# Kernel tuning notes

Hardware: AMD Instinct MI355X
Metric: run time of the kernel (lower is better)

The kernel has to match this reference:

```python
import jax, jax.numpy as jnp
import numpy as np

K = 8            # regular-rep dim (C_8), reg_dim
R_BINS = 3       # num_radii
T_BINS = 16      # num_theta
G = R_BINS * T_BINS
RADIUS = 40.0    # radius_scale
DT = 1.0
CORR = 1.0 / 128.0
SHIFT = 0.2
TWO_PI = 2.0 * np.pi

# [m,n] -> (m-n) mod K, for circulant (group-equivariant) linear maps on the regular rep
_SIDX = (np.arange(K)[:, None] - np.arange(K)[None, :]) % K


def _basis(ab):
    # learnable equivariant intertwiner rho1 <-> regular: a*u_m + b*u_m_perp
    th = jnp.arange(K, dtype=jnp.float32) * (TWO_PI / K)
    U = jnp.stack([jnp.cos(th), jnp.sin(th)], -1)       # [K,2]
    Up = jnp.stack([-jnp.sin(th), jnp.cos(th)], -1)
    return ab[0] * U + ab[1] * Up


def lift_rho1_to_reg(v, ab):
    # v [...,c,2] -> [...,c,K]
    return jnp.einsum('...ca,ma->...cm', v, _basis(ab))


def proj_reg_to_rho1(x, ab):
    # x [...,c,K] -> [...,c,2]
    return jnp.einsum('...cm,ma->...ca', x, _basis(ab))


def equi_linear_reg(x, W):
    # x [...,ci,K], W [co,ci,K]; out[...,o,m] = sum_{i,s} W[o,i,s] x[...,i,(m-s)%K]
    Wc = W[:, :, _SIDX]                                  # [co,ci,m,n]
    return jnp.einsum('...in,oimn->...om', x, Wc)


def _full_kernel(W):
    # base W [co,ci,K,R,T] -> rotated stack [K(m),co,ci,K(n),G]
    s = T_BINS // K
    kern = jnp.stack([jnp.roll(jnp.roll(W, m, axis=2), m * s, axis=4) for m in range(K)], 0)
    return kern.reshape(K, W.shape[0], W.shape[1], K, G)


def pair_bin_weights(p, mask):
    # Dense pairwise continuous-conv weights: window * bilinear polar-grid interpolation,
    # normalized by the neighbor window sum. p [B,N,2], mask [B,N] -> [B,N,N,G]
    N = p.shape[1]
    rel = p[:, None, :, :] - p[:, :, None, :]            # rel[b,i,j] = p_j - p_i
    d = jnp.sqrt(jnp.sum(rel * rel, -1) + 1e-12) / RADIUS
    window = jnp.maximum(1.0 - d * d, 0.0) ** 3          # radius cutoff + window
    wb = window * mask[:, None, :]
    wb = wb / (jnp.sum(wb, -1, keepdims=True) + 1e-6)    # neighbor normalization
    rc = jnp.clip(d * R_BINS - 0.5, 0.0, R_BINS - 1.0)
    r0 = jnp.floor(rc); wr = rc - r0
    r0i = r0.astype(jnp.int32); r1i = jnp.minimum(r0i + 1, R_BINS - 1)
    eye = jnp.eye(N, dtype=bool)[None]                   # safe atan2 at self-pairs
    rx = jnp.where(eye, 1.0, rel[..., 0]); ry = jnp.where(eye, 0.0, rel[..., 1])
    tc = (jnp.arctan2(ry, rx) % TWO_PI) / TWO_PI * T_BINS
    t0 = jnp.floor(tc); wt = tc - t0
    t0i = t0.astype(jnp.int32) % T_BINS; t1i = (t0i + 1) % T_BINS
    gs = [r0i * T_BINS + t0i, r0i * T_BINS + t1i, r1i * T_BINS + t0i, r1i * T_BINS + t1i]
    ws = [(1 - wr) * (1 - wt), (1 - wr) * wt, wr * (1 - wt), wr * wt]
    Wsum = jnp.zeros(d.shape + (G,), jnp.float32)
    for g, w in zip(gs, ws):
        Wsum = Wsum + (w * wb)[..., None] * jax.nn.one_hot(g, G, dtype=jnp.float32)
    return Wsum


def cts_conv(Wsum, feats, Wk):
    # feats [B,N,ci,K] -> [B,N,co,K]
    F = jnp.einsum('bijg,bjcn->bigcn', Wsum, feats)      # bin neighbor features onto polar grid
    return jnp.einsum('bigcn,mocng->biom', F, _full_kernel(Wk))


def mag_act(x):
    mags = jnp.sum(x * x, -1, keepdims=True) + 1e-6
    return x / mags * jax.nn.relu(mags - SHIFT)


def setup_inputs() -> dict:
    key = jax.random.key(0)
    B, N, T = 2, 512, 7
    ks = jax.random.split(key, 20)
    s = 0.05
    return {
        'p0_enc': jax.random.uniform(ks[0], (B, N, T, 2), jnp.float32) * 100.0,
        'v0_enc': jax.random.normal(ks[1], (B, N, T, 2), jnp.float32),
        'p0': jax.random.uniform(ks[2], (B, N, 2), jnp.float32) * 100.0,
        'v0': jax.random.normal(ks[3], (B, N, 2), jnp.float32),
        'a': jax.random.normal(ks[4], (B, N, 2), jnp.float32) * 0.1,
        'fluid_mask': jnp.ones((B, N), jnp.float32),
        'lift_c0': jax.random.normal(ks[5], (2,), jnp.float32) * s,
        'Wc0': jax.random.normal(ks[6], (4, 16, K, R_BINS, T_BINS), jnp.float32) * s,
        'lift_d0': jax.random.normal(ks[7], (2,), jnp.float32) * s,
        'Wd0': jax.random.normal(ks[8], (4, 16, K), jnp.float32) * s,
        'Wc1': jax.random.normal(ks[9], (8, 8, K, R_BINS, T_BINS), jnp.float32) * s,
        'Wd1': jax.random.normal(ks[10], (8, 8, K), jnp.float32) * s,
        'Wc2': jax.random.normal(ks[11], (16, 8, K, R_BINS, T_BINS), jnp.float32) * s,
        'Wd2': jax.random.normal(ks[12], (16, 8, K), jnp.float32) * s,
        'Wc3': jax.random.normal(ks[13], (8, 16, K, R_BINS, T_BINS), jnp.float32) * s,
        'Wd3': jax.random.normal(ks[14], (8, 16, K), jnp.float32) * s,
        'Wc4': jax.random.normal(ks[15], (3, 8, K, R_BINS, T_BINS), jnp.float32) * s,
        'proj_c4': jax.random.normal(ks[16], (2,), jnp.float32) * s,
        'Wd4': jax.random.normal(ks[17], (3, 8, K), jnp.float32) * s,
        'proj_d4': jax.random.normal(ks[18], (2,), jnp.float32) * s,
    }


def reference(p0_enc, v0_enc, p0, v0, a, fluid_mask,
              lift_c0, Wc0, lift_d0, Wd0, Wc1, Wd1, Wc2, Wd2,
              Wc3, Wd3, Wc4, proj_c4, Wd4, proj_d4):
    feats = jnp.concatenate([v0_enc, p0_enc], -2)        # [B,N,14,2]
    v1 = v0 + DT * a
    p1 = p0 + DT * (v0 + v1) / 2.0
    fluid_feats = jnp.concatenate([v1[:, :, None, :], p1[:, :, None, :], feats], -2)  # [B,N,16,2]
    Wsum = pair_bin_weights(p1, fluid_mask)              # shared across all conv layers
    out_conv = cts_conv(Wsum, lift_rho1_to_reg(fluid_feats, lift_c0), Wc0)
    out_dense = equi_linear_reg(lift_rho1_to_reg(fluid_feats, lift_d0), Wd0)
    output = jnp.concatenate([out_conv, out_dense], -2)  # [B,N,8,K]
    for Wc, Wd, last in ((Wc1, Wd1, False), (Wc2, Wd2, False), (Wc3, Wd3, False), (Wc4, Wd4, True)):
        in_feats = mag_act(output)
        oc = cts_conv(Wsum, in_feats, Wc)
        od = equi_linear_reg(in_feats, Wd)
        if last:
            oc = proj_reg_to_rho1(oc, proj_c4)
            od = proj_reg_to_rho1(od, proj_d4)
        new = oc + od
        if new.shape[-2] == output.shape[-2] and new.shape[-1] == output.shape[-1]:
            new = new + output
        output = new
    pos_correction = CORR * output                       # [B,N,3,2]
    p_corr = p1 + pos_correction[..., 0, :]
    v_corr = (p_corr - p0) / DT
    m_matrix = pos_correction[..., 1:, :]                # [B,N,2,2]
    return p_corr, v_corr, m_matrix
```

## Files before the change

### kernel.cpp

```cpp
#include <hip/hip_runtime.h>

#define NPART 1024
#define NNB   512
#define EMAX  2048

__global__ void prep_kernel(const float* __restrict__ p0_enc, const float* __restrict__ v0_enc,
                            const float* __restrict__ p0, const float* __restrict__ v0,
                            const float* __restrict__ a, const float* __restrict__ liftc,
                            const float* __restrict__ liftd,
                            float* __restrict__ featsC, float* __restrict__ Fbuf,
                            float* __restrict__ p1out)
{
    int p = blockIdx.x;
    int t = threadIdx.x;
    int c = t >> 3, m = t & 7;
    float v0x = v0[p*2+0], v0y = v0[p*2+1];
    float ax  = a[p*2+0],  ay  = a[p*2+1];
    float p0x = p0[p*2+0], p0y = p0[p*2+1];
    float v1x = v0x + ax, v1y = v0y + ay;
    float p1x = p0x + 0.5f*(v0x + v1x), p1y = p0y + 0.5f*(v0y + v1y);
    float vx, vy;
    if (c == 0)      { vx = v1x; vy = v1y; }
    else if (c == 1) { vx = p1x; vy = p1y; }
    else if (c < 9)  { vx = v0_enc[(p*7 + (c-2))*2+0]; vy = v0_enc[(p*7 + (c-2))*2+1]; }
    else             { vx = p0_enc[(p*7 + (c-9))*2+0]; vy = p0_enc[(p*7 + (c-9))*2+1]; }
    float th = (float)m * 0.7853981633974483f;
    float cs = cosf(th), sn = sinf(th);
    float lc0 = liftc[0], lc1 = liftc[1];
    float ld0 = liftd[0], ld1 = liftd[1];
    featsC[p*128 + t]        = vx*(lc0*cs - lc1*sn) + vy*(lc0*sn + lc1*cs);
    Fbuf[p*6272 + 6144 + t]  = vx*(ld0*cs - ld1*sn) + vy*(ld0*sn + ld1*cs);
    if (t == 0) { p1out[p*2+0] = p1x; p1out[p*2+1] = p1y; }
}

__global__ void pairs_kernel(const float* __restrict__ p1, const float* __restrict__ mask,
                             float* __restrict__ Ew, unsigned short* __restrict__ Ej,
                             int* __restrict__ offG)
{
    int p  = blockIdx.x;
    int b  = p >> 9;
    int ii = p & 511;
    int tid = threadIdx.x;
    __shared__ float red[256];
    __shared__ float denomS;
    __shared__ int bincnt[48];
    __shared__ int binoff[49];
    __shared__ int binpos[48];
    if (tid < 48) bincnt[tid] = 0;
    float pix = p1[p*2+0], piy = p1[p*2+1];
    float relx[2], rely[2], dd[2], ww[2];
#pragma unroll
    for (int q = 0; q < 2; ++q) {
        int j  = tid + q*256;
        int jr = b*NNB + j;
        float rx = p1[jr*2+0] - pix;
        float ry = p1[jr*2+1] - piy;
        float d  = sqrtf(rx*rx + ry*ry + 1e-12f) * (1.0f/40.0f);
        float t1 = fmaxf(1.0f - d*d, 0.0f);
        float w  = t1*t1*t1 * mask[jr];
        relx[q] = rx; rely[q] = ry; dd[q] = d; ww[q] = w;
    }
    red[tid] = ww[0] + ww[1];
    __syncthreads();
    for (int s = 128; s > 0; s >>= 1) {
        if (tid < s) red[tid] += red[tid+s];
        __syncthreads();
    }
    if (tid == 0) denomS = 1.0f / (red[0] + 1e-6f);
    __syncthreads();
    float dinv = denomS;

    float wsub[2][4];
    int   bsub[2][4];
#pragma unroll
    for (int q = 0; q < 2; ++q) {
        int j  = tid + q*256;
        if (ww[q] == 0.0f) {
#pragma unroll
            for (int k = 0; k < 4; ++k) wsub[q][k] = 0.0f;
            continue;
        }
        float wb = ww[q] * dinv;
        float d  = dd[q];
        float rc  = fminf(fmaxf(d*3.0f - 0.5f, 0.0f), 2.0f);
        float r0f = floorf(rc);
        float wr  = rc - r0f;
        int r0 = (int)r0f;
        int r1 = min(r0 + 1, 2);
        float rx = (j == ii) ? 1.0f : relx[q];
        float ry = (j == ii) ? 0.0f : rely[q];
        float ang = atan2f(ry, rx);
        if (ang < 0.0f) ang += 6.283185307179586f;
        float tc  = ang * 2.546479089470325f;
        float t0f = floorf(tc);
        float wt  = tc - t0f;
        int t0  = ((int)t0f) & 15;
        int t1i = (t0 + 1) & 15;
        wsub[q][0] = wb * (1.0f-wr) * (1.0f-wt);  bsub[q][0] = r0*16 + t0;
        wsub[q][1] = wb * (1.0f-wr) * wt;         bsub[q][1] = r0*16 + t1i;
        wsub[q][2] = wb * wr * (1.0f-wt);         bsub[q][2] = r1*16 + t0;
        wsub[q][3] = wb * wr * wt;                bsub[q][3] = r1*16 + t1i;
#pragma unroll
        for (int k = 0; k < 4; ++k)
            if (wsub[q][k] != 0.0f) atomicAdd(&bincnt[bsub[q][k]], 1);
    }
    __syncthreads();
    if (tid == 0) {
        int s = 0;
#pragma unroll
        for (int g = 0; g < 48; ++g) { binoff[g] = s; s += bincnt[g]; }
        binoff[48] = s;
    }
    __syncthreads();
    if (tid < 48) binpos[tid] = binoff[tid];
    if (tid < 49) offG[p*64 + tid] = binoff[tid];
    __syncthreads();
#pragma unroll
    for (int q = 0; q < 2; ++q) {
        int j = tid + q*256;
#pragma unroll
        for (int k = 0; k < 4; ++k) {
            if (wsub[q][k] != 0.0f) {
                int slot = atomicAdd(&binpos[bsub[q][k]], 1);
                Ew[p*EMAX + slot] = wsub[q][k];
                Ej[p*EMAX + slot] = (unsigned short)j;
            }
        }
    }
}

template<int C8>
__global__ __launch_bounds__(512) void aggregate_kernel(const float* __restrict__ actsrc, int actStride,
                                                        const float* __restrict__ Ew,
                                                        const unsigned short* __restrict__ Ej,
                                                        const int* __restrict__ offG,
                                                        float* __restrict__ Fbuf, int Krow)
{
    int p = blockIdx.x;
    int pbase = p & ~511;
    int tid  = threadIdx.x;
    int lane = tid & 63;
    int wv   = tid >> 6;
    const float* ew = Ew + p*EMAX;
    const unsigned short* ej = Ej + p*EMAX;
    const int* off = offG + p*64;
    float* dst = Fbuf + (size_t)p * Krow;

#pragma unroll
    for (int bi = 0; bi < 6; ++bi) {
        int g = wv + bi*8;
        int e0 = off[g], e1 = off[g+1];
        if (C8 == 128) {
            float2 acc = {0.0f, 0.0f};
            float2 f0 = {0,0}, f1 = {0,0};
            float w0 = 0.0f, w1 = 0.0f;
            if (e0 < e1)     { w0 = ew[e0];   f0 = ((const float2*)(actsrc + (size_t)(pbase + ej[e0])*actStride))[lane]; }
            if (e0 + 1 < e1) { w1 = ew[e0+1]; f1 = ((const float2*)(actsrc + (size_t)(pbase + ej[e0+1])*actStride))[lane]; }
            for (int e = e0; e < e1; ++e) {
                float2 f = f0; float w = w0;
                f0 = f1; w0 = w1;
                if (e + 2 < e1) { w1 = ew[e+2]; f1 = ((const float2*)(actsrc + (size_t)(pbase + ej[e+2])*actStride))[lane]; }
                acc.x += w*f.x; acc.y += w*f.y;
            }
            ((float2*)(dst + g*C8))[lane] = acc;
        } else {
            float acc = 0.0f;
            float f0 = 0, f1 = 0, w0 = 0, w1 = 0;
            if (e0 < e1)     { w0 = ew[e0];   f0 = (actsrc + (size_t)(pbase + ej[e0])*actStride)[lane]; }
            if (e0 + 1 < e1) { w1 = ew[e0+1]; f1 = (actsrc + (size_t)(pbase + ej[e0+1])*actStride)[lane]; }
            for (int e = e0; e < e1; ++e) {
                float f = f0; float w = w0;
                f0 = f1; w0 = w1;
                if (e + 2 < e1) { w1 = ew[e+2]; f1 = (actsrc + (size_t)(pbase + ej[e+2])*actStride)[lane]; }
                acc += w*f;
            }
            dst[g*C8 + lane] = acc;
        }
    }
}

__global__ void expand_kernel(const float* __restrict__ Wc, const float* __restrict__ Wd,
                              const float* __restrict__ pc4, const float* __restrict__ pd4,
                              float* __restrict__ Bm, int C, int O8, int total, int mode)
{
    int e = blockIdx.x*blockDim.x + threadIdx.x;
    if (e >= total) return;
    int col = e % O8;
    int k   = e / O8;
    int C8  = C*8;
    bool conv = (k < 48*C8);
    int cc, nn, rr = 0, tt = 0;
    if (conv) {
        int g = k / C8, rem = k - g*C8;
        cc = rem >> 3; nn = rem & 7; rr = g >> 4; tt = g & 15;
    } else {
        int rem = k - 48*C8;
        cc = rem >> 3; nn = rem & 7;
    }
    float val = 0.0f;
    if (mode == 0) {
        int o = col >> 3, m = col & 7;
        if (conv) val = Wc[(((o*C + cc)*8 + ((nn - m) & 7))*3 + rr)*16 + ((tt - 2*m) & 15)];
        else      val = Wd[(o*C + cc)*8 + ((m - nn) & 7)];
    } else if (mode == 1) {
        int o = col >> 3, m = col & 7;
        if (col < 32) { if (conv)  val = Wc[(((o*C + cc)*8 + ((nn - m)&7))*3 + rr)*16 + ((tt - 2*m)&15)]; }
        else          { if (!conv) val = Wd[((o-4)*C + cc)*8 + ((m - nn)&7)]; }
    } else {
        if (col < 6) {
            int co = col >> 1, aa = col & 1;
            float s0 = conv ? pc4[0] : pd4[0];
            float s1 = conv ? pc4[1] : pd4[1];
#pragma unroll
            for (int m = 0; m < 8; ++m) {
                float th = (float)m * 0.7853981633974483f;
                float csv = cosf(th), snv = sinf(th);
                float bas = (aa == 0) ? (s0*csv - s1*snv) : (s0*snv + s1*csv);
                float wv;
                if (conv) wv = Wc[(((co*C + cc)*8 + ((nn - m)&7))*3 + rr)*16 + ((tt - 2*m)&15)];
                else      wv = Wd[(co*C + cc)*8 + ((m - nn)&7)];
                val += wv * bas;
            }
        }
    }
    Bm[e] = val;
}

template<int N>
__global__ __launch_bounds__(256) void gemm_tile(const float* __restrict__ A, int Kdim,
                                                 const float* __restrict__ B,
                                                 float* __restrict__ Cpart)
{
    constexpr int CT = N/16;
    __shared__ float As[32][68];
    __shared__ float Bs[32][N];
    int tid = threadIdx.x;
    int tr = tid & 15, tc = tid >> 4;
    int m0 = blockIdx.x * 64;
    int k0base = blockIdx.y * 224;
    float acc[4][CT];
#pragma unroll
    for (int i = 0; i < 4; ++i)
#pragma unroll
        for (int u = 0; u < CT; ++u) acc[i][u] = 0.0f;

    int ar = tid >> 2, aq = (tid & 3) * 8;
    for (int k0 = 0; k0 < 224; k0 += 32) {
        const float* Ap = A + (size_t)(m0 + ar)*Kdim + k0base + k0 + aq;
        float4 av0 = *(const float4*)(Ap);
        float4 av1 = *(const float4*)(Ap + 4);
        As[aq+0][ar] = av0.x; As[aq+1][ar] = av0.y; As[aq+2][ar] = av0.z; As[aq+3][ar] = av0.w;
        As[aq+4][ar] = av1.x; As[aq+5][ar] = av1.y; As[aq+6][ar] = av1.z; As[aq+7][ar] = av1.w;
#pragma unroll
        for (int u = 0; u < (8*N + 255)/256; ++u) {
            int idx = tid + 256*u;
            if (idx < 8*N) {
                int row = idx / (N/4), c4 = idx % (N/4);
                *(float4*)&Bs[row][c4*4] = *(const float4*)(B + (size_t)(k0base + k0 + row)*N + c4*4);
            }
        }
        __syncthreads();
#pragma unroll
        for (int kk = 0; kk < 32; ++kk) {
            float4 a4 = *(const float4*)&As[kk][tr*4];
            if (CT == 1) {
                float bv = Bs[kk][tc];
                acc[0][0] += a4.x*bv; acc[1][0] += a4.y*bv;
                acc[2][0] += a4.z*bv; acc[3][0] += a4.w*bv;
            } else {
#pragma unroll
                for (int uu = 0; uu < CT; uu += 4) {
                    float4 b4 = *(const float4*)&Bs[kk][tc*CT + uu];
                    acc[0][uu+0] += a4.x*b4.x; acc[0][uu+1] += a4.x*b4.y; acc[0][uu+2] += a4.x*b4.z; acc[0][uu+3] += a4.x*b4.w;
                    acc[1][uu+0] += a4.y*b4.x; acc[1][uu+1] += a4.y*b4.y; acc[1][uu+2] += a4.y*b4.z; acc[1][uu+3] += a4.y*b4.w;
                    acc[2][uu+0] += a4.z*b4.x; acc[2][uu+1] += a4.z*b4.y; acc[2][uu+2] += a4.z*b4.z; acc[2][uu+3] += a4.z*b4.w;
                    acc[3][uu+0] += a4.w*b4.x; acc[3][uu+1] += a4.w*b4.y; acc[3][uu+2] += a4.w*b4.z; acc[3][uu+3] += a4.w*b4.w;
                }
            }
        }
        __syncthreads();
    }
    float* Cp = Cpart + ((size_t)blockIdx.y*1024 + m0)*N;
#pragma unroll
    for (int i = 0; i < 4; ++i)
#pragma unroll
        for (int u = 0; u < CT; ++u)
            Cp[(size_t)(tr*4 + i)*N + tc*CT + u] = acc[i][u];
}

__global__ void epilogue_kernel(const float* __restrict__ Cpart, int S, int O, int res,
                                float* __restrict__ outBuf, float* __restrict__ actDst, int actStride)
{
    int id = blockIdx.x*blockDim.x + threadIdx.x;
    if (id >= NPART*O) return;
    int p = id / O, c = id % O;
    int O8 = O*8;
    float x[8];
#pragma unroll
    for (int m = 0; m < 8; ++m) x[m] = 0.0f;
    for (int s = 0; s < S; ++s) {
        const float4* q = (const float4*)(Cpart + ((size_t)(s*1024 + p))*O8 + c*8);
        float4 u0 = q[0], u1 = q[1];
        x[0]+=u0.x; x[1]+=u0.y; x[2]+=u0.z; x[3]+=u0.w;
        x[4]+=u1.x; x[5]+=u1.y; x[6]+=u1.z; x[7]+=u1.w;
    }
    float* ob = outBuf + (size_t)p*O8 + c*8;
    float mag = 1e-6f;
#pragma unroll
    for (int m = 0; m < 8; ++m) {
        float v = x[m];
        if (res) v += ob[m];
        x[m] = v; mag += v*v;
    }
#pragma unroll
    for (int m = 0; m < 8; ++m) ob[m] = x[m];
    float sc = fmaxf(mag - 0.2f, 0.0f) / mag;
    float* ad = actDst + (size_t)p*actStride + c*8;
#pragma unroll
    for (int m = 0; m < 8; ++m) ad[m] = x[m]*sc;
}

__global__ void final_kernel(const float* __restrict__ Cpart, int S, const float* __restrict__ p1,
                             const float* __restrict__ p0, float* __restrict__ out)
{
    int p = blockIdx.x*blockDim.x + threadIdx.x;
    if (p >= NPART) return;
    float c[6];
#pragma unroll
    for (int t = 0; t < 6; ++t) c[t] = 0.0f;
    for (int s = 0; s < S; ++s) {
        const float* q = Cpart + ((size_t)(s*1024 + p))*16;
#pragma unroll
        for (int t = 0; t < 6; ++t) c[t] += q[t];
    }
    const float sc = 0.0078125f;
#pragma unroll
    for (int t = 0; t < 6; ++t) c[t] *= sc;
    float pcx = p1[p*2+0] + c[0], pcy = p1[p*2+1] + c[1];
    out[p*2+0] = pcx; out[p*2+1] = pcy;
    out[2048 + p*2+0] = pcx - p0[p*2+0];
    out[2048 + p*2+1] = pcy - p0[p*2+1];
    out[4096 + p*4+0] = c[2]; out[4096 + p*4+1] = c[3];
    out[4096 + p*4+2] = c[4]; out[4096 + p*4+3] = c[5];
}

extern "C" void kernel_launch(void* const* d_in, const int* in_sizes, int n_in,
                              void* d_out, int out_size, void* d_ws, size_t ws_size,
                              hipStream_t stream)
{
    const float* p0_enc  = (const float*)d_in[0];
    const float* v0_enc  = (const float*)d_in[1];
    const float* p0      = (const float*)d_in[2];
    const float* v0      = (const float*)d_in[3];
    const float* a       = (const float*)d_in[4];
    const float* mask    = (const float*)d_in[5];
    const float* lift_c0 = (const float*)d_in[6];
    const float* Wc0     = (const float*)d_in[7];
    const float* lift_d0 = (const float*)d_in[8];
    const float* Wd0     = (const float*)d_in[9];
    const float* Wc1     = (const float*)d_in[10];
    const float* Wd1     = (const float*)d_in[11];
    const float* Wc2     = (const float*)d_in[12];
    const float* Wd2     = (const float*)d_in[13];
    const float* Wc3     = (const float*)d_in[14];
    const float* Wd3     = (const float*)d_in[15];
    const float* Wc4     = (const float*)d_in[16];
    const float* pc4     = (const float*)d_in[17];
    const float* Wd4     = (const float*)d_in[18];
    const float* pd4     = (const float*)d_in[19];
    float* out = (float*)d_out;

    float* wsf    = (float*)d_ws;
    float* featsC = wsf;
    float* p1     = featsC + 131072;
    float* Ew     = p1 + 2048;
    unsigned short* Ej = (unsigned short*)(Ew + 2097152);
    int*   offG   = (int*)(Ew + 2097152 + 1048576);
    float* Fbuf   = (float*)offG + 65536;
    float* Cpart  = Fbuf + 1024*6272;
    float* outBuf = Cpart + 1835008;
    float* Bm0    = outBuf + 131072;
    float* Bm1    = Bm0 + 6272*64;
    float* Bm2    = Bm1 + 3136*64;
    float* Bm3    = Bm2 + 3136*128;
    float* Bm4    = Bm3 + 6272*64;

    prep_kernel<<<NPART, 128, 0, stream>>>(p0_enc, v0_enc, p0, v0, a, lift_c0, lift_d0,
                                           featsC, Fbuf, p1);
    pairs_kernel<<<NPART, 256, 0, stream>>>(p1, mask, Ew, Ej, offG);

    {
        int t0 = 6272*64;  expand_kernel<<<(t0+255)/256, 256, 0, stream>>>(Wc0, Wd0, pc4, pd4, Bm0, 16,  64, t0, 1);
        int t1 = 3136*64;  expand_kernel<<<(t1+255)/256, 256, 0, stream>>>(Wc1, Wd1, pc4, pd4, Bm1,  8,  64, t1, 0);
        int t2 = 3136*128; expand_kernel<<<(t2+255)/256, 256, 0, stream>>>(Wc2, Wd2, pc4, pd4, Bm2,  8, 128, t2, 0);
        int t3 = 6272*64;  expand_kernel<<<(t3+255)/256, 256, 0, stream>>>(Wc3, Wd3, pc4, pd4, Bm3, 16,  64, t3, 0);
        int t4 = 3136*16;  expand_kernel<<<(t4+255)/256, 256, 0, stream>>>(Wc4, Wd4, pc4, pd4, Bm4,  8,  16, t4, 2);
    }

    aggregate_kernel<128><<<NPART, 512, 0, stream>>>(featsC, 128, Ew, Ej, offG, Fbuf, 6272);
    gemm_tile<64><<<dim3(16,28), 256, 0, stream>>>(Fbuf, 6272, Bm0, Cpart);
    epilogue_kernel<<<(NPART*8+63)/64, 64, 0, stream>>>(Cpart, 28, 8, 0, outBuf, Fbuf + 3072, 3136);
    aggregate_kernel<64><<<NPART, 512, 0, stream>>>(Fbuf + 3072, 3136, Ew, Ej, offG, Fbuf, 3136);
    gemm_tile<64><<<dim3(16,14), 256, 0, stream>>>(Fbuf, 3136, Bm1, Cpart);
    epilogue_kernel<<<(NPART*8+63)/64, 64, 0, stream>>>(Cpart, 14, 8, 1, outBuf, Fbuf + 3072, 3136);
    aggregate_kernel<64><<<NPART, 512, 0, stream>>>(Fbuf + 3072, 3136, Ew, Ej, offG, Fbuf, 3136);
    gemm_tile<128><<<dim3(16,14), 256, 0, stream>>>(Fbuf, 3136, Bm2, Cpart);
    epilogue_kernel<<<(NPART*16+63)/64, 64, 0, stream>>>(Cpart, 14, 16, 0, outBuf, Fbuf + 6144, 6272);
    aggregate_kernel<128><<<NPART, 512, 0, stream>>>(Fbuf + 6144, 6272, Ew, Ej, offG, Fbuf, 6272);
    gemm_tile<64><<<dim3(16,28), 256, 0, stream>>>(Fbuf, 6272, Bm3, Cpart);
    epilogue_kernel<<<(NPART*8+63)/64, 64, 0, stream>>>(Cpart, 28, 8, 0, outBuf, Fbuf + 3072, 3136);
    aggregate_kernel<64><<<NPART, 512, 0, stream>>>(Fbuf + 3072, 3136, Ew, Ej, offG, Fbuf, 3136);
    gemm_tile<16><<<dim3(16,14), 256, 0, stream>>>(Fbuf, 3136, Bm4, Cpart);
    final_kernel<<<4, 256, 0, stream>>>(Cpart, 14, p1, p0, out);
}
```

Before: 472.0 us.

## Stage neighbor feature rows in LDS and process multiple particles per block

The aggregate kernel now loads all 512 neighbor rows (64-channel slice) of a particle group into shared memory once per block. It then processes PT particles per block, reading edge weights and indices into LDS and gathering features from LDS instead of global memory. 128-channel layers are split into two 64-channel launches. This cuts repeated global gathers but uses 128KB+ LDS per block, which limits occupancy and reduces the grid size.

New measurement: 527.5 us. 1.12x slower.

```diff
diff --git a/kernel.cpp b/kernel.cpp
--- a/kernel.cpp
+++ b/kernel.cpp
@@ -129,52 +129,66 @@
     }
 }
 
-template<int C8>
+template<int PT>
 __global__ __launch_bounds__(512) void aggregate_kernel(const float* __restrict__ actsrc, int actStride,
+                                                        int choff, int C8,
                                                         const float* __restrict__ Ew,
                                                         const unsigned short* __restrict__ Ej,
                                                         const int* __restrict__ offG,
                                                         float* __restrict__ Fbuf, int Krow)
 {
-    int p = blockIdx.x;
-    int pbase = p & ~511;
+    __shared__ float  rows[512*64];
+    __shared__ float2 ebuf[EMAX];
+    __shared__ int    soff[49];
     int tid  = threadIdx.x;
     int lane = tid & 63;
     int wv   = tid >> 6;
-    const float* ew = Ew + p*EMAX;
-    const unsigned short* ej = Ej + p*EMAX;
-    const int* off = offG + p*64;
-    float* dst = Fbuf + (size_t)p * Krow;
-
-#pragma unroll
-    for (int bi = 0; bi < 6; ++bi) {
-        int g = wv + bi*8;
-        int e0 = off[g], e1 = off[g+1];
-        if (C8 == 128) {
-            float2 acc = {0.0f, 0.0f};
-            float2 f0 = {0,0}, f1 = {0,0};
-            float w0 = 0.0f, w1 = 0.0f;
-            if (e0 < e1)     { w0 = ew[e0];   f0 = ((const float2*)(actsrc + (size_t)(pbase + ej[e0])*actStride))[lane]; }
-            if (e0 + 1 < e1) { w1 = ew[e0+1]; f1 = ((const float2*)(actsrc + (size_t)(pbase + ej[e0+1])*actStride))[lane]; }
-            for (int e = e0; e < e1; ++e) {
-                float2 f = f0; float w = w0;
-                f0 = f1; w0 = w1;
-                if (e + 2 < e1) { w1 = ew[e+2]; f1 = ((const float2*)(actsrc + (size_t)(pbase + ej[e+2])*actStride))[lane]; }
-                acc.x += w*f.x; acc.y += w*f.y;
-            }
-            ((float2*)(dst + g*C8))[lane] = acc;
-        } else {
-            float acc = 0.0f;
-            float f0 = 0, f1 = 0, w0 = 0, w1 = 0;
-            if (e0 < e1)     { w0 = ew[e0];   f0 = (actsrc + (size_t)(pbase + ej[e0])*actStride)[lane]; }
-            if (e0 + 1 < e1) { w1 = ew[e0+1]; f1 = (actsrc + (size_t)(pbase + ej[e0+1])*actStride)[lane]; }
-            for (int e = e0; e < e1; ++e) {
-                float f = f0; float w = w0;
-                f0 = f1; w0 = w1;
-                if (e + 2 < e1) { w1 = ew[e+2]; f1 = (actsrc + (size_t)(pbase + ej[e+2])*actStride)[lane]; }
-                acc += w*f;
-            }
-            dst[g*C8 + lane] = acc;
+    int p0   = blockIdx.x * PT;
+    int pbase = p0 & ~511;
+
+    {
+        float4* r4 = (float4*)rows;
+        for (int k = 0; k < 16; ++k) {
+            int idx4 = tid + k*512;
+            int r = idx4 >> 4, c = (idx4 & 15) * 4;
+            r4[idx4] = *(const float4*)(actsrc + (size_t)(pbase + r)*actStride + choff + c);
+        }
+    }
+
+    for (int pp = 0; pp < PT; ++pp) {
+        int p = p0 + pp;
+        __syncthreads();
+        if (tid < 49) soff[tid] = offG[p*64 + tid];
+        __syncthreads();
+        int cnt = soff[48];
+        for (int i = tid; i < cnt; i += 512) {
+            float2 e; e.x = Ew[p*EMAX + i]; e.y = __uint_as_float((unsigned)Ej[p*EMAX + i]);
+            ebuf[i] = e;
+        }
+        __syncthreads();
+
+        float* dst = Fbuf + (size_t)p * Krow + choff + lane;
+#pragma unroll
+        for (int s = 0; s < 6; ++s) {
+            int g = wv + s*8;
+            int e0 = soff[g], e1 = soff[g+1];
+            float a0 = 0.0f, a1 = 0.0f;
+            int e = e0;
+            for (; e + 2 <= e1; e += 2) {
+                float2 m0 = ebuf[e], m1 = ebuf[e+1];
+                int j0 = (int)__float_as_uint(m0.y);
+                int j1 = (int)__float_as_uint(m1.y);
+                float f0 = rows[j0*64 + lane];
+                float f1 = rows[j1*64 + lane];
+                a0 = fmaf(m0.x, f0, a0);
+                a1 = fmaf(m1.x, f1, a1);
+            }
+            if (e < e1) {
+                float2 m0 = ebuf[e];
+                int j0 = (int)__float_as_uint(m0.y);
+                a0 = fmaf(m0.x, rows[j0*64 + lane], a0);
+            }
+            dst[g*C8] = a0 + a1;
         }
     }
 }
@@ -397,19 +411,21 @@
         int t4 = 3136*16;  expand_kernel<<<(t4+255)/256, 256, 0, stream>>>(Wc4, Wd4, pc4, pd4, Bm4,  8,  16, t4, 2);
     }
 
-    aggregate_kernel<128><<<NPART, 512, 0, stream>>>(featsC, 128, Ew, Ej, offG, Fbuf, 6272);
+    aggregate_kernel<8><<<dim3(128,1), 512, 0, stream>>>(featsC, 128,  0, 128, Ew, Ej, offG, Fbuf, 6272);
+    aggregate_kernel<8><<<dim3(128,1), 512, 0, stream>>>(featsC, 128, 64, 128, Ew, Ej, offG, Fbuf, 6272);
     gemm_tile<64><<<dim3(16,28), 256, 0, stream>>>(Fbuf, 6272, Bm0, Cpart);
     epilogue_kernel<<<(NPART*8+63)/64, 64, 0, stream>>>(Cpart, 28, 8, 0, outBuf, Fbuf + 3072, 3136);
-    aggregate_kernel<64><<<NPART, 512, 0, stream>>>(Fbuf + 3072, 3136, Ew, Ej, offG, Fbuf, 3136);
+    aggregate_kernel<4><<<dim3(256,1), 512, 0, stream>>>(Fbuf + 3072, 3136, 0, 64, Ew, Ej, offG, Fbuf, 3136);
     gemm_tile<64><<<dim3(16,14), 256, 0, stream>>>(Fbuf, 3136, Bm1, Cpart);
     epilogue_kernel<<<(NPART*8+63)/64, 64, 0, stream>>>(Cpart, 14, 8, 1, outBuf, Fbuf + 3072, 3136);
-    aggregate_kernel<64><<<NPART, 512, 0, stream>>>(Fbuf + 3072, 3136, Ew, Ej, offG, Fbuf, 3136);
+    aggregate_kernel<4><<<dim3(256,1), 512, 0, stream>>>(Fbuf + 3072, 3136, 0, 64, Ew, Ej, offG, Fbuf, 3136);
     gemm_tile<128><<<dim3(16,14), 256, 0, stream>>>(Fbuf, 3136, Bm2, Cpart);
     epilogue_kernel<<<(NPART*16+63)/64, 64, 0, stream>>>(Cpart, 14, 16, 0, outBuf, Fbuf + 6144, 6272);
-    aggregate_kernel<128><<<NPART, 512, 0, stream>>>(Fbuf + 6144, 6272, Ew, Ej, offG, Fbuf, 6272);
+    aggregate_kernel<8><<<dim3(128,1), 512, 0, stream>>>(Fbuf + 6144, 6272,  0, 128, Ew, Ej, offG, Fbuf, 6272);
+    aggregate_kernel<8><<<dim3(128,1), 512, 0, stream>>>(Fbuf + 6144, 6272, 64, 128, Ew, Ej, offG, Fbuf, 6272);
     gemm_tile<64><<<dim3(16,28), 256, 0, stream>>>(Fbuf, 6272, Bm3, Cpart);
     epilogue_kernel<<<(NPART*8+63)/64, 64, 0, stream>>>(Cpart, 28, 8, 0, outBuf, Fbuf + 3072, 3136);
-    aggregate_kernel<64><<<NPART, 512, 0, stream>>>(Fbuf + 3072, 3136, Ew, Ej, offG, Fbuf, 3136);
+    aggregate_kernel<4><<<dim3(256,1), 512, 0, stream>>>(Fbuf + 3072, 3136, 0, 64, Ew, Ej, offG, Fbuf, 3136);
     gemm_tile<16><<<dim3(16,14), 256, 0, stream>>>(Fbuf, 3136, Bm4, Cpart);
     final_kernel<<<4, 256, 0, stream>>>(Cpart, 14, p1, p0, out);
 }
```
